# Performance work log

Hardware: AMD Instinct MI355X
Metric: run time of the kernel (lower is better)

## Reference

```python
import jax, jax.numpy as jnp
import numpy as np

B, T, DIN, DC, CS = 8, 4096, 1024, 256, 8192
EPS = 1e-12

def _l2norm(x):
    # F.normalize: x / max(||x||_2, eps) along last axis
    n = jnp.sqrt(jnp.sum(x * x, axis=-1, keepdims=True))
    return x / jnp.maximum(n, EPS)

def _wn(v, g):
    # torch weight_norm(dim=0): w = g * v / ||v|| per output row
    n = jnp.sqrt(jnp.sum(v * v, axis=1, keepdims=True))
    return g * v / jnp.maximum(n, EPS)

def setup_inputs() -> dict:
    key = jax.random.key(0)
    k = jax.random.split(key, 4)
    return {
        "z": jax.random.normal(k[0], (B, DIN, T), jnp.float32),
        "in_v": jax.random.normal(k[1], (DC, DIN), jnp.float32) * 0.02,
        "in_g": jnp.ones((DC, 1), jnp.float32),
        "in_b": jnp.zeros((DC,), jnp.float32),
        "out_v": jax.random.normal(k[2], (DIN, DC), jnp.float32) * 0.02,
        "out_g": jnp.ones((DIN, 1), jnp.float32),
        "out_b": jnp.zeros((DIN,), jnp.float32),
        "codebook": jax.random.normal(k[3], (CS, DC), jnp.float32),
    }

def reference(z, in_v, in_g, in_b, out_v, out_g, out_b, codebook):
    b, _, t = z.shape
    w_in = _wn(in_v, in_g)                      # (DC, DIN)
    z_e = jnp.einsum('bdt,cd->bct', z, w_in) + in_b[None, :, None]  # (B, DC, T)

    # decode_latents (eval mode: dropout p=0)
    enc = _l2norm(z_e.transpose(0, 2, 1).reshape(b * t, -1))   # (BT, DC)
    cb = _l2norm(codebook)                                     # (CS, DC)
    dist = (jnp.sum(enc * enc, axis=1, keepdims=True)
            - 2.0 * enc @ cb.T
            + jnp.sum(cb * cb, axis=1)[None, :])               # (BT, CS)
    indices = jnp.argmax(-dist, axis=1).reshape(b, t)          # (B, T)
    z_q = codebook[indices].transpose(0, 2, 1)                 # (B, DC, T)

    commitment_loss = jnp.mean((z_e - jax.lax.stop_gradient(z_q)) ** 2, axis=(1, 2))
    codebook_loss = jnp.mean((z_q - jax.lax.stop_gradient(z_e)) ** 2, axis=(1, 2))

    z_q_st = z_e + jax.lax.stop_gradient(z_q - z_e)            # straight-through
    w_out = _wn(out_v, out_g)                                  # (DIN, DC)
    z_q_out = jnp.einsum('bct,dc->bdt', z_q_st, w_out) + out_b[None, :, None]
    return (z_q_out, commitment_loss, codebook_loss, indices)
```

## Files before the change

### kernel.cpp

```cpp
#include <hip/hip_runtime.h>
#include <stdint.h>

#define BB 8
#define TT 4096
#define DIN 1024
#define DC 256
#define CS 8192
#define EPSF 1e-12f

typedef unsigned short ushort_t;
typedef __attribute__((ext_vector_type(8))) short short8;
typedef __attribute__((ext_vector_type(4))) float f32x4;

constexpr size_t OFF_WIN   = 0;
constexpr size_t OFF_WOUTT = OFF_WIN   + 1048576;
constexpr size_t OFF_CBN   = OFF_WOUTT + 1048576;
constexpr size_t OFF_NRM2  = OFF_CBN   + 8388608;
constexpr size_t OFF_ZE    = OFF_NRM2  + 32768;
constexpr size_t OFF_INV   = OFF_ZE    + 33554432;
constexpr size_t OFF_ENC2  = OFF_INV   + 131072;
constexpr size_t OFF_KEYS  = OFF_ENC2  + 131072;
constexpr size_t OFF_LOSS  = OFF_KEYS  + 262144;
constexpr size_t OFF_WSPL  = OFF_LOSS  + 256;
constexpr size_t OFF_W2T   = OFF_WSPL  + 1048576;
constexpr size_t REQ_WS_ZE = OFF_W2T + 134217728ull;

__device__ __forceinline__ float block_reduce_sum_256(float v, float* sbuf) {
  #pragma unroll
  for (int o = 32; o > 0; o >>= 1) v += __shfl_down(v, o, 64);
  int lane = threadIdx.x & 63, w = threadIdx.x >> 6;
  if (lane == 0) sbuf[w] = v;
  __syncthreads();
  float r = sbuf[0] + sbuf[1] + sbuf[2] + sbuf[3];
  __syncthreads();
  return r;
}

__device__ __forceinline__ ushort_t bf16_rne(float x) {
  unsigned u = __float_as_uint(x);
  unsigned r = (u + 0x7FFFu + ((u >> 16) & 1u)) >> 16;
  return (ushort_t)r;
}
__device__ __forceinline__ float bf16f(ushort_t h) {
  return __uint_as_float(((unsigned)h) << 16);
}

__device__ __forceinline__ int swz4(int r) {
  return (r + (r >> 2)) & 3;
}

__device__ __forceinline__ void async_copy16(const ushort_t* g, ushort_t* lds) {
  __builtin_amdgcn_global_load_lds(
      (const __attribute__((address_space(1))) void*)g,
      (__attribute__((address_space(3))) void*)lds, 16, 0, 0);
}

__device__ __forceinline__ void stage_tile8(const ushort_t* __restrict__ s0,
                                            ushort_t* __restrict__ dstbuf,
                                            const int (&go)[8]) {
  #pragma unroll
  for (int i = 0; i < 8; i++) async_copy16(s0 + go[i], dstbuf + i*512);
}

__device__ __forceinline__ void stage2(const ushort_t* __restrict__ srcbase,
                                       ushort_t* __restrict__ comp,
                                       const int (&go)[2], int wu) {
  async_copy16(srcbase + go[0], comp + wu);
  async_copy16(srcbase + go[1], comp + wu + 4096);
}

#define LD8(base, off) (*(const short8*)((const char*)(base) + (off)))

template<int MH, int CLO>
__device__ __forceinline__ void qmfma(f32x4 (&acc)[8][4],
    const short8 (&fah)[4], const short8 (&fal)[4],
    const short8 (&fbh)[4], const short8 (&fbl)[4]) {
  #pragma unroll
  for (int r = 0; r < 4; r++) {
    #pragma unroll
    for (int c2 = 0; c2 < 2; c2++) {
      f32x4 t = acc[MH*4 + r][CLO + c2];
      t = __builtin_amdgcn_mfma_f32_16x16x32_bf16(fah[r], fbh[CLO + c2], t, 0, 0, 0);
      t = __builtin_amdgcn_mfma_f32_16x16x32_bf16(fal[r], fbh[CLO + c2], t, 0, 0, 0);
      t = __builtin_amdgcn_mfma_f32_16x16x32_bf16(fah[r], fbl[CLO + c2], t, 0, 0, 0);
      acc[MH*4 + r][CLO + c2] = t;
    }
  }
}

__global__ void k_prep_win(const float* __restrict__ v, const float* __restrict__ g,
                           float* __restrict__ w, ushort_t* __restrict__ wh,
                           ushort_t* __restrict__ wl) {
  __shared__ float sb[4];
  int r = blockIdx.x, t = threadIdx.x;
  float xv[4]; float s = 0.f;
  #pragma unroll
  for (int i = 0; i < 4; i++) { xv[i] = v[r*DIN + t + i*256]; s += xv[i]*xv[i]; }
  s = block_reduce_sum_256(s, sb);
  float sc = g[r] / fmaxf(sqrtf(s), EPSF);
  #pragma unroll
  for (int i = 0; i < 4; i++) {
    float val = xv[i] * sc;
    int idx = r*DIN + t + i*256;
    w[idx] = val;
    ushort_t h = bf16_rne(val);
    wh[idx] = h;
    wl[idx] = bf16_rne(val - bf16f(h));
  }
}

__global__ void k_prep_wout(const float* __restrict__ v, const float* __restrict__ g,
                            float* __restrict__ wT) {
  __shared__ float sb[4];
  int r = blockIdx.x, t = threadIdx.x;
  float x = v[r*DC + t];
  float s = block_reduce_sum_256(x*x, sb);
  float sc = g[r] / fmaxf(sqrtf(s), EPSF);
  wT[t*DIN + r] = x * sc;
}

__global__ void k_prep_cb(const float* __restrict__ cb, ushort_t* __restrict__ cbh,
                          ushort_t* __restrict__ cbl, float* __restrict__ nrm2) {
  __shared__ float sb[4];
  int j = blockIdx.x, t = threadIdx.x;
  float x = cb[j*DC + t];
  float s = block_reduce_sum_256(x*x, sb);
  float nm = fmaxf(sqrtf(s), EPSF);
  float cn = x / nm;
  ushort_t h = bf16_rne(cn);
  cbh[j*DC + t] = h;
  cbl[j*DC + t] = bf16_rne(cn - bf16f(h));
  float q = block_reduce_sum_256(cn*cn, sb);
  if (t == 0) nrm2[j] = q;
}

__global__ void k_split_cbraw(const float* __restrict__ cb, ushort_t* __restrict__ ch,
                              ushort_t* __restrict__ cl) {
  int j = blockIdx.x, t = threadIdx.x;
  float x = cb[j*DC + t];
  ushort_t h = bf16_rne(x);
  ch[j*DC + t] = h;
  cl[j*DC + t] = bf16_rne(x - bf16f(h));
}

__global__ void k_split_wout(const float* __restrict__ v, const float* __restrict__ g,
                             ushort_t* __restrict__ wh, ushort_t* __restrict__ wl) {
  __shared__ float sb[4];
  int r = blockIdx.x, t = threadIdx.x;
  float x = v[r*DC + t];
  float s = block_reduce_sum_256(x*x, sb);
  float sc = g[r] / fmaxf(sqrtf(s), EPSF);
  float val = x * sc;
  ushort_t h = bf16_rne(val);
  wh[r*DC + t] = h;
  wl[r*DC + t] = bf16_rne(val - bf16f(h));
}

template<bool BIAS>
__global__ __launch_bounds__(256) void k_gemm(
    const float* __restrict__ A, const float* __restrict__ Bmat,
    const float* __restrict__ bias, float* __restrict__ C,
    int K, int lda, int ldb, int ldc, size_t strideB, size_t strideC)
{
  __shared__ float As[16][132];
  __shared__ float Bs[16][132];
  const int bn = blockIdx.x * 128;
  const int bm = blockIdx.y * 128;
  const float* Bb = Bmat + (size_t)blockIdx.z * strideB;
  float* Cb = C + (size_t)blockIdx.z * strideC;
  const int tid = threadIdx.x;
  const int tx = tid & 15, ty = tid >> 4;
  const int am = tid & 127, akq = (tid >> 7) * 8;
  const int bk = tid >> 5, bj = (tid & 31) * 4;

  float acc[8][8];
  #pragma unroll
  for (int i = 0; i < 8; i++)
    #pragma unroll
    for (int j = 0; j < 8; j++) acc[i][j] = 0.f;

  for (int k0 = 0; k0 < K; k0 += 16) {
    float4 a0 = *(const float4*)&A[(size_t)(bm+am)*lda + k0 + akq];
    float4 a1 = *(const float4*)&A[(size_t)(bm+am)*lda + k0 + akq + 4];
    float4 b0 = *(const float4*)&Bb[(size_t)(k0+bk)*ldb + bn + bj];
    float4 b1 = *(const float4*)&Bb[(size_t)(k0+bk+8)*ldb + bn + bj];
    As[akq+0][am] = a0.x; As[akq+1][am] = a0.y; As[akq+2][am] = a0.z; As[akq+3][am] = a0.w;
    As[akq+4][am] = a1.x; As[akq+5][am] = a1.y; As[akq+6][am] = a1.z; As[akq+7][am] = a1.w;
    *(float4*)&Bs[bk][bj] = b0;
    *(float4*)&Bs[bk+8][bj] = b1;
    __syncthreads();
    #pragma unroll
    for (int k = 0; k < 16; k++) {
      float av[8], bv[8];
      float4 x0 = *(const float4*)&As[k][tx*4];
      float4 x1 = *(const float4*)&As[k][tx*4+64];
      float4 y0 = *(const float4*)&Bs[k][ty*4];
      float4 y1 = *(const float4*)&Bs[k][ty*4+64];
      av[0]=x0.x; av[1]=x0.y; av[2]=x0.z; av[3]=x0.w;
      av[4]=x1.x; av[5]=x1.y; av[6]=x1.z; av[7]=x1.w;
      bv[0]=y0.x; bv[1]=y0.y; bv[2]=y0.z; bv[3]=y0.w;
      bv[4]=y1.x; bv[5]=y1.y; bv[6]=y1.z; bv[7]=y1.w;
      #pragma unroll
      for (int i = 0; i < 8; i++)
        #pragma unroll
        for (int j = 0; j < 8; j++)
          acc[i][j] += av[i] * bv[j];
    }
    __syncthreads();
  }

  #pragma unroll
  for (int i = 0; i < 8; i++) {
    int mm = bm + ((i < 4) ? tx*4 + i : 64 + tx*4 + (i-4));
    float bia = BIAS ? bias[mm] : 0.f;
    float4 v0 = make_float4(acc[i][0]+bia, acc[i][1]+bia, acc[i][2]+bia, acc[i][3]+bia);
    float4 v1 = make_float4(acc[i][4]+bia, acc[i][5]+bia, acc[i][6]+bia, acc[i][7]+bia);
    *(float4*)&Cb[(size_t)mm*ldc + bn + ty*4]      = v0;
    *(float4*)&Cb[(size_t)mm*ldc + bn + 64 + ty*4] = v1;
  }
}

__global__ void k_split_z(const float* __restrict__ z, ushort_t* __restrict__ zhi,
                          ushort_t* __restrict__ zlo) {
  __shared__ float tile[64][65];
  int b = blockIdx.z, t0 = blockIdx.x * 64, d0 = blockIdx.y * 64;
  int tx = threadIdx.x & 63, ty = threadIdx.x >> 6;
  const float* zb = z + (size_t)b*DIN*TT;
  #pragma unroll
  for (int i = 0; i < 16; i++) {
    int d = i*4 + ty;
    tile[d][tx] = zb[(size_t)(d0+d)*TT + t0 + tx];
  }
  __syncthreads();
  #pragma unroll
  for (int i = 0; i < 16; i++) {
    int t = i*4 + ty;
    float val = tile[tx][t];
    ushort_t h = bf16_rne(val);
    size_t o = ((size_t)(b*TT + t0 + t))*DIN + d0 + tx;
    zhi[o] = h;
    zlo[o] = bf16_rne(val - bf16f(h));
  }
}

__global__ __launch_bounds__(256) void k_ze_mfma(
    const ushort_t* __restrict__ zth, const ushort_t* __restrict__ ztl,
    const ushort_t* __restrict__ wh, const ushort_t* __restrict__ wl,
    const float* __restrict__ in_b, float* __restrict__ ze)
{
  __shared__ ushort_t As_hi[2][4096];
  __shared__ ushort_t As_lo[2][4096];
  __shared__ ushort_t Bs_hi[2][4096];
  __shared__ ushort_t Bs_lo[2][4096];

  const int b  = blockIdx.z;
  const int t0 = blockIdx.x * 128;
  const int c0 = blockIdx.y * 128;
  const int tid = threadIdx.x;
  const int lane = tid & 63;
  const int wave = tid >> 6;
  const int wr = wave >> 1, wc = wave & 1;
  const int m = lane & 15, quad = lane >> 4;

  const ushort_t* src; ushort_t* dst;
  {
    size_t aoff = ((size_t)(b*TT + t0)) * DIN;
    size_t boff = (size_t)c0 * DIN;
    if      (wave == 0) { src = zth + aoff; dst = &As_hi[0][0]; }
    else if (wave == 1) { src = ztl + aoff; dst = &As_lo[0][0]; }
    else if (wave == 2) { src = wh + boff;  dst = &Bs_hi[0][0]; }
    else                { src = wl + boff;  dst = &Bs_lo[0][0]; }
  }
  const int rr = lane >> 2, cc = lane & 3;

  int goT[8];
  #pragma unroll
  for (int i = 0; i < 8; i++) {
    int r = i*16 + rr;
    int g = cc ^ swz4(r);
    goT[i] = r*DIN + (g << 3);
  }

  int offA[4], offB[4];
  #pragma unroll
  for (int ri = 0; ri < 4; ri++) {
    int r = wr*64 + ri*16 + m;
    int p = quad ^ swz4(r);
    offA[ri] = r*64 + p*16;
  }
  #pragma unroll
  for (int ci = 0; ci < 4; ci++) {
    int r = wc*64 + ci*16 + m;
    int p = quad ^ swz4(r);
    offB[ci] = r*64 + p*16;
  }

  f32x4 acc[4][4];
  #pragma unroll
  for (int i = 0; i < 4; i++)
    #pragma unroll
    for (int j = 0; j < 4; j++) acc[i][j] = (f32x4)0.f;

  stage_tile8(src, dst, goT);

  for (int it = 0; it < 32; ++it) {
    __syncthreads();
    if (it < 31) stage_tile8(src + (it+1)*32, dst + ((it+1)&1)*4096, goT);
    const int bo = (it & 1) << 13;

    short8 bh[4], bl[4];
    #pragma unroll
    for (int ci = 0; ci < 4; ci++) {
      bh[ci] = *(const short8*)((const char*)Bs_hi + bo + offB[ci]);
      bl[ci] = *(const short8*)((const char*)Bs_lo + bo + offB[ci]);
    }
    #pragma unroll
    for (int ri = 0; ri < 4; ri++) {
      short8 ah = *(const short8*)((const char*)As_hi + bo + offA[ri]);
      short8 al = *(const short8*)((const char*)As_lo + bo + offA[ri]);
      #pragma unroll
      for (int ci = 0; ci < 4; ci++) {
        acc[ri][ci] = __builtin_amdgcn_mfma_f32_16x16x32_bf16(ah, bh[ci], acc[ri][ci], 0, 0, 0);
        acc[ri][ci] = __builtin_amdgcn_mfma_f32_16x16x32_bf16(al, bh[ci], acc[ri][ci], 0, 0, 0);
        acc[ri][ci] = __builtin_amdgcn_mfma_f32_16x16x32_bf16(ah, bl[ci], acc[ri][ci], 0, 0, 0);
      }
    }
  }

  #pragma unroll
  for (int ri = 0; ri < 4; ri++) {
    int t_loc = wr*64 + ri*16 + quad*4;
    #pragma unroll
    for (int ci = 0; ci < 4; ci++) {
      int c_loc = wc*64 + ci*16 + m;
      float bia = in_b[c0 + c_loc];
      float4 v = make_float4(acc[ri][ci][0]+bia, acc[ri][ci][1]+bia,
                             acc[ri][ci][2]+bia, acc[ri][ci][3]+bia);
      *(float4*)&ze[((size_t)b*DC + c0 + c_loc)*TT + t0 + t_loc] = v;
    }
  }
}

__global__ __launch_bounds__(256) void k_w2t_mfma(
    const ushort_t* __restrict__ ah_g, const ushort_t* __restrict__ al_g,
    const ushort_t* __restrict__ bh_g, const ushort_t* __restrict__ bl_g,
    float* __restrict__ C)
{
  __shared__ ushort_t As_hi[2][4096];
  __shared__ ushort_t As_lo[2][4096];
  __shared__ ushort_t Bs_hi[2][4096];
  __shared__ ushort_t Bs_lo[2][4096];

  const int m0 = blockIdx.x * 128;
  const int n0 = blockIdx.y * 128;
  const int tid = threadIdx.x;
  const int lane = tid & 63;
  const int wave = tid >> 6;
  const int wr = wave >> 1, wc = wave & 1;
  const int m = lane & 15, quad = lane >> 4;

  const ushort_t* src; ushort_t* dst;
  {
    size_t aoff = (size_t)m0 * DC;
    size_t boff = (size_t)n0 * DC;
    if      (wave == 0) { src = ah_g + aoff; dst = &As_hi[0][0]; }
    else if (wave == 1) { src = al_g + aoff; dst = &As_lo[0][0]; }
    else if (wave == 2) { src = bh_g + boff; dst = &Bs_hi[0][0]; }
    else                { src = bl_g + boff; dst = &Bs_lo[0][0]; }
  }
  const int rr = lane >> 2, cc = lane & 3;

  int goT[8];
  #pragma unroll
  for (int i = 0; i < 8; i++) {
    int r = i*16 + rr;
    int g = cc ^ swz4(r);
    goT[i] = r*DC + (g << 3);
  }

  int offA[4], offB[4];
  #pragma unroll
  for (int ri = 0; ri < 4; ri++) {
    int r = wr*64 + ri*16 + m;
    int p = quad ^ swz4(r);
    offA[ri] = r*64 + p*16;
  }
  #pragma unroll
  for (int ci = 0; ci < 4; ci++) {
    int r = wc*64 + ci*16 + m;
    int p = quad ^ swz4(r);
    offB[ci] = r*64 + p*16;
  }

  f32x4 acc[4][4];
  #pragma unroll
  for (int i = 0; i < 4; i++)
    #pragma unroll
    for (int j = 0; j < 4; j++) acc[i][j] = (f32x4)0.f;

  stage_tile8(src, dst, goT);

  for (int it = 0; it < 8; ++it) {
    __syncthreads();
    if (it < 7) stage_tile8(src + (it+1)*32, dst + ((it+1)&1)*4096, goT);
    const int bo = (it & 1) << 13;

    short8 bh[4], bl[4];
    #pragma unroll
    for (int ci = 0; ci < 4; ci++) {
      bh[ci] = *(const short8*)((const char*)Bs_hi + bo + offB[ci]);
      bl[ci] = *(const short8*)((const char*)Bs_lo + bo + offB[ci]);
    }
    #pragma unroll
    for (int ri = 0; ri < 4; ri++) {
      short8 ah = *(const short8*)((const char*)As_hi + bo + offA[ri]);
      short8 al = *(const short8*)((const char*)As_lo + bo + offA[ri]);
      #pragma unroll
      for (int ci = 0; ci < 4; ci++) {
        acc[ri][ci] = __builtin_amdgcn_mfma_f32_16x16x32_bf16(ah, bh[ci], acc[ri][ci], 0, 0, 0);
        acc[ri][ci] = __builtin_amdgcn_mfma_f32_16x16x32_bf16(al, bh[ci], acc[ri][ci], 0, 0, 0);
        acc[ri][ci] = __builtin_amdgcn_mfma_f32_16x16x32_bf16(ah, bl[ci], acc[ri][ci], 0, 0, 0);
      }
    }
  }

  #pragma unroll
  for (int ri = 0; ri < 4; ri++) {
    int m_loc = wr*64 + ri*16 + quad*4;
    #pragma unroll
    for (int ci = 0; ci < 4; ci++) {
      int n_loc = wc*64 + ci*16 + m;
      #pragma unroll
      for (int reg = 0; reg < 4; reg++) {
        C[(size_t)(m0 + m_loc + reg)*DIN + n0 + n_loc] = acc[ri][ci][reg];
      }
    }
  }
}

__global__ void k_colnorm(const float* __restrict__ ze, float* __restrict__ inv,
                          float* __restrict__ enc2) {
  int r = blockIdx.x * 256 + threadIdx.x;
  int b = r >> 12, t = r & 4095;
  const float* p = ze + (size_t)b*DC*TT + t;
  float s = 0.f;
  for (int c = 0; c < DC; c++) { float x = p[(size_t)c*TT]; s += x*x; }
  float iv = 1.f / fmaxf(sqrtf(s), EPSF);
  inv[r] = iv;
  enc2[r] = (s * iv) * iv;
}

__global__ void k_split_enc(const float* __restrict__ ze, const float* __restrict__ inv,
                            ushort_t* __restrict__ ehi, ushort_t* __restrict__ elo) {
  __shared__ float tile[64][65];
  int b = blockIdx.z, t0 = blockIdx.x * 64, c0 = blockIdx.y * 64;
  int tx = threadIdx.x & 63, ty = threadIdx.x >> 6;
  const float* zb = ze + (size_t)b*DC*TT;
  #pragma unroll
  for (int i = 0; i < 16; i++) {
    int c = i*4 + ty;
    tile[c][tx] = zb[(size_t)(c0+c)*TT + t0 + tx];
  }
  __syncthreads();
  #pragma unroll
  for (int i = 0; i < 16; i++) {
    int t = i*4 + ty;
    float iv = inv[b*TT + t0 + t];
    float val = tile[tx][t] * iv;
    ushort_t h = bf16_rne(val);
    size_t o = ((size_t)(b*TT + t0 + t))*DC + c0 + tx;
    ehi[o] = h;
    elo[o] = bf16_rne(val - bf16f(h));
  }
}

__global__ __launch_bounds__(512, 2) void k_dist_mfma(
    const ushort_t* __restrict__ ehi, const ushort_t* __restrict__ elo,
    const ushort_t* __restrict__ cbh, const ushort_t* __restrict__ cbl,
    const float* __restrict__ nrm2, const float* __restrict__ enc2,
    unsigned long long* __restrict__ keys)
{
  __shared__ ushort_t sAh[2][8192];
  __shared__ ushort_t sAl[2][8192];
  __shared__ ushort_t sBh[2][8192];
  __shared__ ushort_t sBl[2][8192];
  __shared__ float sE2[256], sN2[256];
  __shared__ unsigned long long rkey[256];

  const int j0 = blockIdx.x * 256;
  const size_t r0 = (size_t)blockIdx.y * 256;
  const int tid = threadIdx.x;
  const int lane = tid & 63;
  const int wave = tid >> 6;
  const int wr = wave >> 2, wc = wave & 3;
  const int ml = lane & 15, quad = lane >> 4;

  if (tid < 256) {
    sE2[tid] = enc2[r0 + tid];
    sN2[tid] = nrm2[j0 + tid];
    rkey[tid] = 0xFFFFFFFFFFFFFFFFull;
  }

  const ushort_t* gAh = ehi + r0 * DC;
  const ushort_t* gAl = elo + r0 * DC;
  const ushort_t* gBh = cbh + (size_t)j0 * DC;
  const ushort_t* gBl = cbl + (size_t)j0 * DC;

  int goS[2];
  #pragma unroll
  for (int l = 0; l < 2; l++) {
    int chunk = l*512 + tid;
    int r = chunk >> 2, c = chunk & 3;
    int g = c ^ swz4(r);
    goS[l] = r*DC + (g << 3);
  }
  const int wu = wave * 512;

  int offA[8], offB[4];
  #pragma unroll
  for (int i = 0; i < 8; i++) {
    int r = wr*128 + i*16 + ml;
    int p = quad ^ swz4(r);
    offA[i] = r*64 + p*16;
  }
  #pragma unroll
  for (int i = 0; i < 4; i++) {
    int r = wc*64 + i*16 + ml;
    int p = quad ^ swz4(r);
    offB[i] = r*64 + p*16;
  }

  f32x4 acc[8][4];
  #pragma unroll
  for (int i = 0; i < 8; i++)
    #pragma unroll
    for (int j = 0; j < 4; j++) acc[i][j] = (f32x4)0.f;

  stage2(gBh,      &sBh[0][0], goS, wu);
  stage2(gBl,      &sBl[0][0], goS, wu);
  stage2(gAh,      &sAh[0][0], goS, wu);
  stage2(gAl,      &sAl[0][0], goS, wu);
  stage2(gBh + 32, &sBh[1][0], goS, wu);
  stage2(gBl + 32, &sBl[1][0], goS, wu);
  asm volatile("s_waitcnt vmcnt(4)" ::: "memory");
  asm volatile("s_waitcnt lgkmcnt(0)" ::: "memory");
  __builtin_amdgcn_s_barrier();
  __builtin_amdgcn_sched_barrier(0);

  short8 fa_h[4], fa_l[4], fb_h[4], fb_l[4];

  #pragma unroll 2
  for (int k = 0; k < 8; k++) {
    const int cb = k & 1, nb = cb ^ 1;
    const char* pAh = (const char*)&sAh[cb][0];
    const char* pAl = (const char*)&sAl[cb][0];
    const char* pBh = (const char*)&sBh[cb][0];
    const char* pBl = (const char*)&sBl[cb][0];
    __builtin_amdgcn_sched_barrier(0);

    #pragma unroll
    for (int i = 0; i < 4; i++) { fa_h[i] = LD8(pAh, offA[i]); fa_l[i] = LD8(pAl, offA[i]); }
    #pragma unroll
    for (int i = 0; i < 2; i++) { fb_h[i] = LD8(pBh, offB[i]); fb_l[i] = LD8(pBl, offB[i]); }
    if (k < 7) stage2(gAh + (size_t)(k+1)*32, &sAh[nb][0], goS, wu);
    __builtin_amdgcn_s_barrier();
    __builtin_amdgcn_s_setprio(1);
    qmfma<0, 0>(acc, fa_h, fa_l, fb_h, fb_l);
    __builtin_amdgcn_s_setprio(0);
    __builtin_amdgcn_s_barrier();

    #pragma unroll
    for (int i = 2; i < 4; i++) { fb_h[i] = LD8(pBh, offB[i]); fb_l[i] = LD8(pBl, offB[i]); }
    if (k < 7) stage2(gAl + (size_t)(k+1)*32, &sAl[nb][0], goS, wu);
    __builtin_amdgcn_s_barrier();
    __builtin_amdgcn_s_setprio(1);
    qmfma<0, 2>(acc, fa_h, fa_l, fb_h, fb_l);
    __builtin_amdgcn_s_setprio(0);
    __builtin_amdgcn_s_barrier();

    #pragma unroll
    for (int i = 0; i < 4; i++) { fa_h[i] = LD8(pAh, offA[4+i]); fa_l[i] = LD8(pAl, offA[4+i]); }
    if (k < 6) {
      stage2(gBh + (size_t)(k+2)*32, &sBh[cb][0], goS, wu);
      stage2(gBl + (size_t)(k+2)*32, &sBl[cb][0], goS, wu);
    }
    __builtin_amdgcn_s_barrier();
    __builtin_amdgcn_s_setprio(1);
    qmfma<1, 2>(acc, fa_h, fa_l, fb_h, fb_l);
    qmfma<1, 0>(acc, fa_h, fa_l, fb_h, fb_l);
    __builtin_amdgcn_s_setprio(0);
    if (k < 6) { asm volatile("s_waitcnt vmcnt(4)" ::: "memory"); }
    else       { asm volatile("s_waitcnt vmcnt(0)" ::: "memory"); }
    __builtin_amdgcn_s_barrier();
  }

  #pragma unroll
  for (int ri = 0; ri < 8; ri++) {
    #pragma unroll
    for (int reg = 0; reg < 4; reg++) {
      int t_loc = wr*128 + ri*16 + quad*4 + reg;
      float e2 = sE2[t_loc];
      unsigned long long best = 0xFFFFFFFFFFFFFFFFull;
      #pragma unroll
      for (int ci = 0; ci < 4; ci++) {
        int j_loc = wc*64 + ci*16 + ml;
        float d = e2 - 2.0f * acc[ri][ci][reg];
        d = d + sN2[j_loc];
        unsigned long long key =
            ((unsigned long long)__float_as_uint(d) << 32) | (unsigned)(j0 + j_loc);
        best = key < best ? key : best;
      }
      #pragma unroll
      for (int off = 1; off < 16; off <<= 1) {
        unsigned long long o = __shfl_xor(best, off);
        best = o < best ? o : best;
      }
      if (ml == 0) atomicMin(&rkey[t_loc], best);
    }
  }
  __syncthreads();
  if (tid < 256) atomicMin(&keys[r0 + tid], rkey[tid]);
}

__global__ void k_lossidx(const float* __restrict__ ze, const float* __restrict__ cb,
                          const unsigned long long* __restrict__ keys,
                          float* __restrict__ loss_sums, float* __restrict__ out_idx)
{
  __shared__ float sb[4];
  __shared__ int sj[64];
  int b = blockIdx.y, t0 = blockIdx.x * 64;
  int tid = threadIdx.x;
  if (tid < 64) {
    unsigned long long k = keys[(size_t)b*TT + t0 + tid];
    int j = (int)(unsigned)(k & 0xFFFFFFFFull);
    sj[tid] = j;
    out_idx[(size_t)b*TT + t0 + tid] = (float)j;
  }
  __syncthreads();
  int tt = tid & 63, tc = tid >> 6;
  const float* zb = ze + (size_t)b*DC*TT + t0;
  int j = sj[tt];
  float s = 0.f;
  for (int ci = 0; ci < 64; ci++) {
    int c = tc + ci*4;
    float zev = zb[(size_t)c*TT + tt];
    float zqv = cb[(size_t)j*DC + c];
    float d = zev - zqv;
    s += d*d;
  }
  s = block_reduce_sum_256(s, sb);
  if (tid == 0) atomicAdd(&loss_sums[b], s);
}

__global__ void k_losswrite(const float* __restrict__ loss_sums, float* __restrict__ out_loss) {
  int i = threadIdx.x;
  if (i < 8) {
    float v = loss_sums[i] * (1.f/1048576.f);
    out_loss[i] = v;
    out_loss[8 + i] = v;
  }
}

__global__ void k_outgather(const float* __restrict__ W2T,
                            const unsigned long long* __restrict__ keys,
                            const float* __restrict__ out_b, float* __restrict__ out)
{
  __shared__ float tile[64][65];
  __shared__ int sj[64];
  int b = blockIdx.y, t0 = blockIdx.x * 64;
  int tid = threadIdx.x;
  if (tid < 64) sj[tid] = (int)(unsigned)(keys[(size_t)b*TT + t0 + tid] & 0xFFFFFFFFull);
  __syncthreads();
  float* ob = out + (size_t)b*DIN*TT;
  int dd = tid & 63, tq = tid >> 6;
  for (int d0 = 0; d0 < DIN; d0 += 64) {
    #pragma unroll
    for (int i = 0; i < 16; i++) {
      int t = tq*16 + i;
      tile[t][dd] = W2T[(size_t)sj[t]*DIN + d0 + dd];
    }
    __syncthreads();
    #pragma unroll
    for (int i = 0; i < 16; i++) {
      int d = tq*16 + i;
      ob[(size_t)(d0+d)*TT + t0 + dd] = tile[dd][d] + out_b[d0+d];
    }
    __syncthreads();
  }
}

extern "C" void kernel_launch(void* const* d_in, const int* in_sizes, int n_in,
                              void* d_out, int out_size, void* d_ws, size_t ws_size,
                              hipStream_t stream) {
  const float* z        = (const float*)d_in[0];
  const float* in_v     = (const float*)d_in[1];
  const float* in_g     = (const float*)d_in[2];
  const float* in_b     = (const float*)d_in[3];
  const float* out_v    = (const float*)d_in[4];
  const float* out_g    = (const float*)d_in[5];
  const float* out_b    = (const float*)d_in[6];
  const float* codebook = (const float*)d_in[7];

  char* w = (char*)d_ws;
  float* w_in   = (float*)(w + OFF_WIN);
  float* w_outT = (float*)(w + OFF_WOUTT);
  ushort_t* cb_hi = (ushort_t*)(w + OFF_CBN);
  ushort_t* cb_lo = cb_hi + (size_t)CS*DC;
  float* nrm2   = (float*)(w + OFF_NRM2);
  float* z_e    = (float*)(w + OFF_ZE);
  float* inv    = (float*)(w + OFF_INV);
  float* enc2   = (float*)(w + OFF_ENC2);
  unsigned long long* keys = (unsigned long long*)(w + OFF_KEYS);
  float* loss_sums = (float*)(w + OFF_LOSS);
  ushort_t* w_hi = (ushort_t*)(w + OFF_WSPL);
  ushort_t* w_lo = w_hi + (size_t)DC*DIN;
  ushort_t* zt_hi = (ushort_t*)(w + OFF_W2T);
  ushort_t* zt_lo = zt_hi + (size_t)BB*TT*DIN;
  ushort_t* enc_hi = (ushort_t*)(w + OFF_W2T);
  ushort_t* enc_lo = enc_hi + (size_t)BB*TT*DC;
  float* W2T    = (float*)(w + OFF_W2T);
  ushort_t* cbr_hi  = (ushort_t*)(w + OFF_W2T + 33554432);
  ushort_t* cbr_lo  = cbr_hi + (size_t)CS*DC;
  ushort_t* wout_hi = (ushort_t*)(w + OFF_W2T + 33554432 + 8388608);
  ushort_t* wout_lo = wout_hi + (size_t)DIN*DC;

  float* out      = (float*)d_out;
  float* out_loss = out + (size_t)BB*DIN*TT;
  float* out_idx  = out_loss + 16;

  hipMemsetAsync(keys, 0xFF, 32768ull*8, stream);
  hipMemsetAsync(loss_sums, 0, 32, stream);

  const bool mfma_path = (ws_size >= REQ_WS_ZE);

  k_prep_win <<<256, 256, 0, stream>>>(in_v, in_g, w_in, w_hi, w_lo);
  k_prep_cb  <<<8192, 256, 0, stream>>>(codebook, cb_hi, cb_lo, nrm2);

  if (mfma_path) {
    k_split_z<<<dim3(64, 16, 8), 256, 0, stream>>>(z, zt_hi, zt_lo);
    k_ze_mfma<<<dim3(32, 2, 8), 256, 0, stream>>>(zt_hi, zt_lo, w_hi, w_lo, in_b, z_e);
  } else {
    k_prep_wout<<<1024, 256, 0, stream>>>(out_v, out_g, w_outT);
    k_gemm<true><<<dim3(32, 2, 8), 256, 0, stream>>>(
        w_in, z, in_b, z_e, 1024, 1024, 4096, 4096,
        (size_t)DIN*TT, (size_t)DC*TT);
  }

  k_colnorm<<<128, 256, 0, stream>>>(z_e, inv, enc2);
  k_split_enc<<<dim3(64, 4, 8), 256, 0, stream>>>(z_e, inv, enc_hi, enc_lo);

  k_dist_mfma<<<dim3(32, 128), 512, 0, stream>>>(
      enc_hi, enc_lo, cb_hi, cb_lo, nrm2, enc2, keys);

  k_lossidx<<<dim3(64, 8), 256, 0, stream>>>(z_e, codebook, keys, loss_sums, out_idx);
  k_losswrite<<<1, 64, 0, stream>>>(loss_sums, out_loss);

  if (mfma_path) {
    k_split_cbraw<<<8192, 256, 0, stream>>>(codebook, cbr_hi, cbr_lo);
    k_split_wout <<<1024, 256, 0, stream>>>(out_v, out_g, wout_hi, wout_lo);
    k_w2t_mfma<<<dim3(64, 8), 256, 0, stream>>>(cbr_hi, cbr_lo, wout_hi, wout_lo, W2T);
  } else {
    k_gemm<false><<<dim3(8, 64, 1), 256, 0, stream>>>(
        codebook, w_outT, nullptr, W2T, 256, 256, 1024, 1024,
        (size_t)0, (size_t)0);
  }

  k_outgather<<<dim3(64, 8), 256, 0, stream>>>(W2T, keys, out_b, out);
}
```

Before: 907.7 us.

## Shrink distance GEMM tiles to 128x128 with simple double-buffered pipeline

```diff
diff --git a/kernel.cpp b/kernel.cpp
--- a/kernel.cpp
+++ b/kernel.cpp
@@ -62,31 +62,14 @@
   for (int i = 0; i < 8; i++) async_copy16(s0 + go[i], dstbuf + i*512);
 }
 
-__device__ __forceinline__ void stage2(const ushort_t* __restrict__ srcbase,
+__device__ __forceinline__ void stageD(const ushort_t* __restrict__ srcbase,
                                        ushort_t* __restrict__ comp,
                                        const int (&go)[2], int wu) {
   async_copy16(srcbase + go[0], comp + wu);
-  async_copy16(srcbase + go[1], comp + wu + 4096);
+  async_copy16(srcbase + go[1], comp + wu + 2048);
 }
 
 #define LD8(base, off) (*(const short8*)((const char*)(base) + (off)))
-
-template<int MH, int CLO>
-__device__ __forceinline__ void qmfma(f32x4 (&acc)[8][4],
-    const short8 (&fah)[4], const short8 (&fal)[4],
-    const short8 (&fbh)[4], const short8 (&fbl)[4]) {
-  #pragma unroll
-  for (int r = 0; r < 4; r++) {
-    #pragma unroll
-    for (int c2 = 0; c2 < 2; c2++) {
-      f32x4 t = acc[MH*4 + r][CLO + c2];
-      t = __builtin_amdgcn_mfma_f32_16x16x32_bf16(fah[r], fbh[CLO + c2], t, 0, 0, 0);
-      t = __builtin_amdgcn_mfma_f32_16x16x32_bf16(fal[r], fbh[CLO + c2], t, 0, 0, 0);
-      t = __builtin_amdgcn_mfma_f32_16x16x32_bf16(fah[r], fbl[CLO + c2], t, 0, 0, 0);
-      acc[MH*4 + r][CLO + c2] = t;
-    }
-  }
-}
 
 __global__ void k_prep_win(const float* __restrict__ v, const float* __restrict__ g,
                            float* __restrict__ w, ushort_t* __restrict__ wh,
@@ -440,7 +423,7 @@
 
 __global__ void k_colnorm(const float* __restrict__ ze, float* __restrict__ inv,
                           float* __restrict__ enc2) {
-  int r = blockIdx.x * 256 + threadIdx.x;
+  int r = blockIdx.x * 128 + threadIdx.x;
   int b = r >> 12, t = r & 4095;
   const float* p = ze + (size_t)b*DC*TT + t;
   float s = 0.f;
@@ -474,28 +457,28 @@
   }
 }
 
-__global__ __launch_bounds__(512, 2) void k_dist_mfma(
+__global__ __launch_bounds__(256, 2) void k_dist_mfma(
     const ushort_t* __restrict__ ehi, const ushort_t* __restrict__ elo,
     const ushort_t* __restrict__ cbh, const ushort_t* __restrict__ cbl,
     const float* __restrict__ nrm2, const float* __restrict__ enc2,
     unsigned long long* __restrict__ keys)
 {
-  __shared__ ushort_t sAh[2][8192];
-  __shared__ ushort_t sAl[2][8192];
-  __shared__ ushort_t sBh[2][8192];
-  __shared__ ushort_t sBl[2][8192];
-  __shared__ float sE2[256], sN2[256];
-  __shared__ unsigned long long rkey[256];
-
-  const int j0 = blockIdx.x * 256;
-  const size_t r0 = (size_t)blockIdx.y * 256;
+  __shared__ ushort_t sAh[2][4096];
+  __shared__ ushort_t sAl[2][4096];
+  __shared__ ushort_t sBh[2][4096];
+  __shared__ ushort_t sBl[2][4096];
+  __shared__ float sE2[128], sN2[128];
+  __shared__ unsigned long long rkey[128];
+
+  const int j0 = blockIdx.x * 128;
+  const size_t r0 = (size_t)blockIdx.y * 128;
   const int tid = threadIdx.x;
   const int lane = tid & 63;
   const int wave = tid >> 6;
-  const int wr = wave >> 2, wc = wave & 3;
+  const int wr = wave >> 1, wc = wave & 1;
   const int ml = lane & 15, quad = lane >> 4;
 
-  if (tid < 256) {
+  if (tid < 128) {
     sE2[tid] = enc2[r0 + tid];
     sN2[tid] = nrm2[j0 + tid];
     rkey[tid] = 0xFFFFFFFFFFFFFFFFull;
@@ -509,17 +492,17 @@
   int goS[2];
   #pragma unroll
   for (int l = 0; l < 2; l++) {
-    int chunk = l*512 + tid;
+    int chunk = l*256 + tid;
     int r = chunk >> 2, c = chunk & 3;
     int g = c ^ swz4(r);
     goS[l] = r*DC + (g << 3);
   }
   const int wu = wave * 512;
 
-  int offA[8], offB[4];
-  #pragma unroll
-  for (int i = 0; i < 8; i++) {
-    int r = wr*128 + i*16 + ml;
+  int offA[4], offB[4];
+  #pragma unroll
+  for (int i = 0; i < 4; i++) {
+    int r = wr*64 + i*16 + ml;
     int p = quad ^ swz4(r);
     offA[i] = r*64 + p*16;
   }
@@ -530,75 +513,59 @@
     offB[i] = r*64 + p*16;
   }
 
-  f32x4 acc[8][4];
-  #pragma unroll
-  for (int i = 0; i < 8; i++)
+  f32x4 acc[4][4];
+  #pragma unroll
+  for (int i = 0; i < 4; i++)
     #pragma unroll
     for (int j = 0; j < 4; j++) acc[i][j] = (f32x4)0.f;
 
-  stage2(gBh,      &sBh[0][0], goS, wu);
-  stage2(gBl,      &sBl[0][0], goS, wu);
-  stage2(gAh,      &sAh[0][0], goS, wu);
-  stage2(gAl,      &sAl[0][0], goS, wu);
-  stage2(gBh + 32, &sBh[1][0], goS, wu);
-  stage2(gBl + 32, &sBl[1][0], goS, wu);
-  asm volatile("s_waitcnt vmcnt(4)" ::: "memory");
-  asm volatile("s_waitcnt lgkmcnt(0)" ::: "memory");
-  __builtin_amdgcn_s_barrier();
-  __builtin_amdgcn_sched_barrier(0);
-
-  short8 fa_h[4], fa_l[4], fb_h[4], fb_l[4];
+  stageD(gAh, &sAh[0][0], goS, wu);
+  stageD(gAl, &sAl[0][0], goS, wu);
+  stageD(gBh, &sBh[0][0], goS, wu);
+  stageD(gBl, &sBl[0][0], goS, wu);
+  __syncthreads();
 
   #pragma unroll 2
-  for (int k = 0; k < 8; k++) {
+  for (int k = 0; k < 8; ++k) {
     const int cb = k & 1, nb = cb ^ 1;
+    if (k < 7) {
+      stageD(gAh + (size_t)(k+1)*32, &sAh[nb][0], goS, wu);
+      stageD(gAl + (size_t)(k+1)*32, &sAl[nb][0], goS, wu);
+      stageD(gBh + (size_t)(k+1)*32, &sBh[nb][0], goS, wu);
+      stageD(gBl + (size_t)(k+1)*32, &sBl[nb][0], goS, wu);
+    }
     const char* pAh = (const char*)&sAh[cb][0];
     const char* pAl = (const char*)&sAl[cb][0];
     const char* pBh = (const char*)&sBh[cb][0];
     const char* pBl = (const char*)&sBl[cb][0];
-    __builtin_amdgcn_sched_barrier(0);
-
-    #pragma unroll
-    for (int i = 0; i < 4; i++) { fa_h[i] = LD8(pAh, offA[i]); fa_l[i] = LD8(pAl, offA[i]); }
-    #pragma unroll
-    for (int i = 0; i < 2; i++) { fb_h[i] = LD8(pBh, offB[i]); fb_l[i] = LD8(pBl, offB[i]); }
-    if (k < 7) stage2(gAh + (size_t)(k+1)*32, &sAh[nb][0], goS, wu);
-    __builtin_amdgcn_s_barrier();
+
+    short8 fah[4], fal[4], fbh[4], fbl[4];
+    #pragma unroll
+    for (int i = 0; i < 4; i++) {
+      fah[i] = LD8(pAh, offA[i]); fal[i] = LD8(pAl, offA[i]);
+      fbh[i] = LD8(pBh, offB[i]); fbl[i] = LD8(pBl, offB[i]);
+    }
     __builtin_amdgcn_s_setprio(1);
-    qmfma<0, 0>(acc, fa_h, fa_l, fb_h, fb_l);
+    #pragma unroll
+    for (int ri = 0; ri < 4; ri++) {
+      #pragma unroll
+      for (int ci = 0; ci < 4; ci++) {
+        f32x4 t = acc[ri][ci];
+        t = __builtin_amdgcn_mfma_f32_16x16x32_bf16(fah[ri], fbh[ci], t, 0, 0, 0);
+        t = __builtin_amdgcn_mfma_f32_16x16x32_bf16(fal[ri], fbh[ci], t, 0, 0, 0);
+        t = __builtin_amdgcn_mfma_f32_16x16x32_bf16(fah[ri], fbl[ci], t, 0, 0, 0);
+        acc[ri][ci] = t;
+      }
+    }
     __builtin_amdgcn_s_setprio(0);
-    __builtin_amdgcn_s_barrier();
-
-    #pragma unroll
-    for (int i = 2; i < 4; i++) { fb_h[i] = LD8(pBh, offB[i]); fb_l[i] = LD8(pBl, offB[i]); }
-    if (k < 7) stage2(gAl + (size_t)(k+1)*32, &sAl[nb][0], goS, wu);
-    __builtin_amdgcn_s_barrier();
-    __builtin_amdgcn_s_setprio(1);
-    qmfma<0, 2>(acc, fa_h, fa_l, fb_h, fb_l);
-    __builtin_amdgcn_s_setprio(0);
-    __builtin_amdgcn_s_barrier();
-
-    #pragma unroll
-    for (int i = 0; i < 4; i++) { fa_h[i] = LD8(pAh, offA[4+i]); fa_l[i] = LD8(pAl, offA[4+i]); }
-    if (k < 6) {
-      stage2(gBh + (size_t)(k+2)*32, &sBh[cb][0], goS, wu);
-      stage2(gBl + (size_t)(k+2)*32, &sBl[cb][0], goS, wu);
-    }
-    __builtin_amdgcn_s_barrier();
-    __builtin_amdgcn_s_setprio(1);
-    qmfma<1, 2>(acc, fa_h, fa_l, fb_h, fb_l);
-    qmfma<1, 0>(acc, fa_h, fa_l, fb_h, fb_l);
-    __builtin_amdgcn_s_setprio(0);
-    if (k < 6) { asm volatile("s_waitcnt vmcnt(4)" ::: "memory"); }
-    else       { asm volatile("s_waitcnt vmcnt(0)" ::: "memory"); }
-    __builtin_amdgcn_s_barrier();
-  }
-
-  #pragma unroll
-  for (int ri = 0; ri < 8; ri++) {
+    __syncthreads();
+  }
+
+  #pragma unroll
+  for (int ri = 0; ri < 4; ri++) {
     #pragma unroll
     for (int reg = 0; reg < 4; reg++) {
-      int t_loc = wr*128 + ri*16 + quad*4 + reg;
+      int t_loc = wr*64 + ri*16 + quad*4 + reg;
       float e2 = sE2[t_loc];
       unsigned long long best = 0xFFFFFFFFFFFFFFFFull;
       #pragma unroll
@@ -619,7 +586,7 @@
     }
   }
   __syncthreads();
-  if (tid < 256) atomicMin(&keys[r0 + tid], rkey[tid]);
+  if (tid < 128) atomicMin(&keys[r0 + tid], rkey[tid]);
 }
 
 __global__ void k_lossidx(const float* __restrict__ ze, const float* __restrict__ cb,
@@ -746,10 +713,10 @@
         (size_t)DIN*TT, (size_t)DC*TT);
   }
 
-  k_colnorm<<<128, 256, 0, stream>>>(z_e, inv, enc2);
+  k_colnorm<<<256, 128, 0, stream>>>(z_e, inv, enc2);
   k_split_enc<<<dim3(64, 4, 8), 256, 0, stream>>>(z_e, inv, enc_hi, enc_lo);
 
-  k_dist_mfma<<<dim3(32, 128), 512, 0, stream>>>(
+  k_dist_mfma<<<dim3(64, 256), 256, 0, stream>>>(
       enc_hi, enc_lo, cb_hi, cb_lo, nrm2, enc2, keys);
 
   k_lossidx<<<dim3(64, 8), 256, 0, stream>>>(z_e, codebook, keys, loss_sums, out_idx);
```

Result: slower. 982.2 us (+8.2%).
